# Performance work log

Measured on AMD Instinct MI355X. Metric: run time of the kernel, lower is better.

## Reference

```python
import jax, jax.numpy as jnp
import numpy as np


def setup_inputs() -> dict:
    key = jax.random.key(0)
    k1, k2, k3, k4 = jax.random.split(key, 4)
    B, C, H, W = 8, 3, 1024, 2048
    M, h, w = 32, H // 8, W // 8
    img = jax.random.uniform(k1, (B, C, H, W), dtype=jnp.float32)
    planar_masks = jax.random.normal(k2, (B, M, h, w), dtype=jnp.float32)
    disp = jax.random.uniform(k3, (B, h, w), dtype=jnp.float32) * 0.9 + 0.1
    K = jnp.array([[721.5, 0.0, w / 2.0], [0.0, 721.5, h / 2.0], [0.0, 0.0, 1.0]], dtype=jnp.float32)
    intrs = jnp.tile(K[None], (B, 1, 1))
    baseline = jax.random.uniform(k4, (B,), dtype=jnp.float32) * 0.4 + 0.3
    return {"img": img, "planar_masks": planar_masks, "disp": disp, "intrs": intrs, "baseline": baseline}


def reference(img, planar_masks, disp, intrs, baseline):
    B, C, H, W = img.shape
    _, M, h, w = planar_masks.shape
    dt = img.dtype

    # disp -> depth (b,h,w)
    focal = (intrs[:, 0, 0] + intrs[:, 1, 1]) * 0.5
    depth = baseline[:, None, None] * focal[:, None, None] / (disp * 2048.0)

    # depth -> normals via 3x3 Sobel-style central differences, zero padding
    dp = jnp.pad(depth, ((0, 0), (1, 1), (1, 1)))
    gx = 0.5 * (dp[:, 1:-1, 2:] - dp[:, 1:-1, :-2])
    gy = 0.5 * (dp[:, 2:, 1:-1] - dp[:, :-2, 1:-1])
    dir_map = jnp.stack([-gx, -gy, jnp.ones_like(gx)], axis=1)  # (B,3,h,w)
    normal = dir_map / jnp.sqrt(jnp.sum(dir_map ** 2, axis=1, keepdims=True))

    # softmax-weighted per-plane depth/normal (faithful torch .view memory layout)
    wts = jax.nn.softmax(planar_masks.reshape(B, M, h * w), axis=-1)  # (B,M,hw)
    flat_depth = depth.reshape(B, h * w, 1)
    flat_normal = normal.reshape(B, h * w, 3)  # channel-major flatten, as in source
    planar_depth = wts @ flat_depth   # (B,M,1)
    planar_normal = wts @ flat_normal  # (B,M,3)

    # per-plane homographies H = K (R - t n^T / d) K^-1
    R = jnp.broadcast_to(jnp.eye(3, dtype=dt), (B, 3, 3))
    t = jnp.zeros((B, 3, 1), dt).at[:, 2, 0].set(-baseline)
    K_inv = jnp.linalg.inv(intrs)
    tn = t[:, None] @ planar_normal[:, :, None, :]            # (B,M,3,3)
    H_cal = R[:, None] - tn / planar_depth[..., None]
    Hm = intrs[:, None] @ H_cal @ K_inv[:, None]              # (B,M,3,3)

    img_p = img.reshape(B, C, h, 8, w, 8).mean(axis=(3, 5))  # (B,C,h,w)

    # affine_grid (align_corners=True) with the top 2 rows of H
    ys = jnp.linspace(-1.0, 1.0, h, dtype=dt)
    xs = jnp.linspace(-1.0, 1.0, w, dtype=dt)
    gyy, gxx = jnp.meshgrid(ys, xs, indexing="ij")
    base = jnp.stack([gxx, gyy, jnp.ones_like(gxx)], axis=-1)  # (h,w,3)
    grid = jnp.einsum("bmij,hwj->bmhwi", Hm[:, :, :2, :], base)  # (B,M,h,w,2)

    # bilinear grid_sample, zeros padding, align_corners=True
    ix = (grid[..., 0] + 1.0) * (w - 1) * 0.5
    iy = (grid[..., 1] + 1.0) * (h - 1) * 0.5
    x0 = jnp.floor(ix)
    y0 = jnp.floor(iy)
    wx1 = ix - x0
    wy1 = iy - y0
    imgT = img_p.transpose(0, 2, 3, 1)  # (B,h,w,C)
    bidx = jnp.arange(B)[:, None, None, None]

    def corner(xf, yf):
        valid = (xf >= 0) & (xf <= w - 1) & (yf >= 0) & (yf <= h - 1)
        xi = jnp.clip(xf, 0, w - 1).astype(jnp.int32)
        yi = jnp.clip(yf, 0, h - 1).astype(jnp.int32)
        return imgT[bidx, yi, xi] * valid[..., None].astype(dt)  # (B,M,h,w,C)

    warp = (corner(x0, y0) * ((1 - wx1) * (1 - wy1))[..., None]
            + corner(x0 + 1, y0) * (wx1 * (1 - wy1))[..., None]
            + corner(x0, y0 + 1) * ((1 - wx1) * wy1)[..., None]
            + corner(x0 + 1, y0 + 1) * (wx1 * wy1)[..., None])  # (B,M,h,w,C)

    blend = jax.nn.softmax(planar_masks, axis=1)  # (B,M,h,w)
    return jnp.einsum("bmhwc,bmhw->bchw", warp, blend)
```

## Files before the change

### kernel.cpp

```cpp
#include <hip/hip_runtime.h>
#include <math.h>

#define Bq   8
#define Cc   3
#define Hh   128
#define Ww   256
#define Mm   32
#define HW   (Hh*Ww)
#define HIMG 1024
#define WIMG 2048

__global__ void k_dn(const float* __restrict__ disp,
                     const float* __restrict__ intrs,
                     const float* __restrict__ baseline,
                     float* __restrict__ depth,
                     float* __restrict__ normal) {
    int idx = blockIdx.x * 256 + threadIdx.x;
    int b = idx >> 15;
    int p = idx & (HW - 1);
    int y = p >> 8;
    int x = p & (Ww - 1);
    float focal = 0.5f * (intrs[b * 9 + 0] + intrs[b * 9 + 4]);
    float k = baseline[b] * focal * (1.0f / 2048.0f);
    const float* db = disp + (size_t)b * HW;
    float Dc  = k / db[p];
    float Dxm = (x > 0)      ? k / db[p - 1]  : 0.0f;
    float Dxp = (x < Ww - 1) ? k / db[p + 1]  : 0.0f;
    float Dym = (y > 0)      ? k / db[p - Ww] : 0.0f;
    float Dyp = (y < Hh - 1) ? k / db[p + Ww] : 0.0f;
    float gx = 0.5f * (Dxp - Dxm);
    float gy = 0.5f * (Dyp - Dym);
    float invn = 1.0f / sqrtf(gx * gx + gy * gy + 1.0f);
    depth[idx] = Dc;
    float* nb = normal + (size_t)b * 3 * HW;
    nb[p]          = -gx * invn;
    nb[HW + p]     = -gy * invn;
    nb[2 * HW + p] =  invn;
}

__global__ __launch_bounds__(512) void k_pool_planes(
        const float* __restrict__ img, float4* __restrict__ img_p,
        const float* __restrict__ masks,
        const float* __restrict__ depth, const float* __restrict__ normal,
        const float* __restrict__ intrs, const float* __restrict__ baseline,
        float* __restrict__ hm) {
    int blk = blockIdx.x;
    int tid = threadIdx.x;
    __shared__ float lds[5][8];
    if (blk < Bq * Mm) {
        int bm = blk;
        int b = bm >> 5;
        const float4* mp = (const float4*)(masks + (size_t)bm * HW);
        const float4* dp = (const float4*)(depth + (size_t)b * HW);
        const float4* np = (const float4*)(normal + (size_t)b * 3 * HW);
        int lane = tid & 63, wid = tid >> 6;

        float se = 0.f, sd = 0.f, s0 = 0.f, s1 = 0.f, s2 = 0.f;
        #pragma unroll 4
        for (int kk = 0; kk < HW / 4 / 512; kk++) {
            int i = tid + kk * 512;
            float4 mk  = mp[i];
            float4 d4  = dp[i];
            float4 n0v = np[3 * i], n1v = np[3 * i + 1], n2v = np[3 * i + 2];
            float e0 = __expf(mk.x), e1 = __expf(mk.y);
            float e2 = __expf(mk.z), e3 = __expf(mk.w);
            se += (e0 + e1) + (e2 + e3);
            sd = fmaf(e0, d4.x, fmaf(e1, d4.y, fmaf(e2, d4.z, fmaf(e3, d4.w, sd))));
            s0 = fmaf(e0, n0v.x, fmaf(e1, n0v.w, fmaf(e2, n1v.z, fmaf(e3, n2v.y, s0))));
            s1 = fmaf(e0, n0v.y, fmaf(e1, n1v.x, fmaf(e2, n1v.w, fmaf(e3, n2v.z, s1))));
            s2 = fmaf(e0, n0v.z, fmaf(e1, n1v.y, fmaf(e2, n2v.x, fmaf(e3, n2v.w, s2))));
        }
        float vals[5] = {se, sd, s0, s1, s2};
        #pragma unroll
        for (int j = 0; j < 5; j++) {
            float v = vals[j];
            #pragma unroll
            for (int off = 32; off; off >>= 1) v += __shfl_down(v, off, 64);
            if (lane == 0) lds[j][wid] = v;
        }
        __syncthreads();

        if (tid == 0) {
            float t[5];
            #pragma unroll
            for (int j = 0; j < 5; j++) {
                float r = 0.f;
                #pragma unroll
                for (int i = 0; i < 8; i++) r += lds[j][i];
                t[j] = r;
            }
            float inv_se = 1.0f / t[0];
            float pd = t[1] * inv_se;
            float n0 = t[2] * inv_se, n1 = t[3] * inv_se, n2 = t[4] * inv_se;
            const float* Km = intrs + b * 9;
            float a = Km[0], bb = Km[1], c = Km[2];
            float d = Km[3], e  = Km[4], f = Km[5];
            float g = Km[6], h2 = Km[7], i = Km[8];
            float det = a * (e * i - f * h2) - bb * (d * i - f * g) + c * (d * h2 - e * g);
            float invd = 1.0f / det;
            float ki[9] = {(e * i - f * h2) * invd, (c * h2 - bb * i) * invd, (bb * f - c * e) * invd,
                           (f * g - d * i) * invd, (a * i - c * g) * invd,  (c * d - a * f) * invd,
                           (d * h2 - e * g) * invd, (bb * g - a * h2) * invd, (a * e - bb * d) * invd};
            float s = baseline[b] / pd;
            float A[9] = {1.f, 0.f, 0.f, 0.f, 1.f, 0.f, s * n0, s * n1, 1.0f + s * n2};
            float T[9];
            #pragma unroll
            for (int r = 0; r < 3; r++)
                #pragma unroll
                for (int cc = 0; cc < 3; cc++)
                    T[r * 3 + cc] = Km[r * 3 + 0] * A[cc] + Km[r * 3 + 1] * A[3 + cc] + Km[r * 3 + 2] * A[6 + cc];
            #pragma unroll
            for (int r = 0; r < 2; r++)
                #pragma unroll
                for (int cc = 0; cc < 3; cc++)
                    hm[bm * 6 + r * 3 + cc] = T[r * 3 + 0] * ki[cc] + T[r * 3 + 1] * ki[3 + cc] + T[r * 3 + 2] * ki[6 + cc];
        }
    } else {
        int pb = blk - Bq * Mm;
        int b = pb >> 6;
        int y = ((pb & 63) << 1) | (tid >> 8);
        int x = tid & 255;
        float s[3];
        #pragma unroll
        for (int c = 0; c < 3; c++) {
            const float* base = img + ((size_t)(b * 3 + c) * HIMG + (size_t)y * 8) * WIMG + x * 8;
            float acc = 0.f;
            #pragma unroll
            for (int r = 0; r < 8; r++) {
                float4 u = *(const float4*)(base + (size_t)r * WIMG);
                float4 v = *(const float4*)(base + (size_t)r * WIMG + 4);
                acc += u.x + u.y + u.z + u.w + v.x + v.y + v.z + v.w;
            }
            s[c] = acc * (1.0f / 64.0f);
        }
        img_p[((size_t)(b * Hh + y)) * Ww + x] = make_float4(s[0], s[1], s[2], 0.f);
    }
}

__global__ __launch_bounds__(512) void k_blend(const float* __restrict__ masks,
                        const float* __restrict__ hm,
                        const float4* __restrict__ img_p,
                        float* __restrict__ out) {
    int bi = blockIdx.x;
    int b = bi >> 7;
    int y = bi & (Hh - 1);
    int tid = threadIdx.x;
    int x = tid & (Ww - 1);
    int half = tid >> 8;
    __shared__ float hs[Mm * 6];
    __shared__ float part[4][Ww];
    if (tid < Mm * 6) hs[tid] = hm[b * Mm * 6 + tid];
    __syncthreads();

    const float* mp = masks + (size_t)b * Mm * HW + (size_t)(half * 16) * HW
                    + (size_t)y * Ww + x;
    float mv[16];
    #pragma unroll
    for (int m = 0; m < 16; m++) mv[m] = mp[(size_t)m * HW];

    float xn = (2.0f * x - (float)(Ww - 1)) * (1.0f / (float)(Ww - 1));
    float yn = (2.0f * y - (float)(Hh - 1)) * (1.0f / (float)(Hh - 1));
    const float4* ip = img_p + (size_t)b * HW;
    const float* hb = hs + half * 16 * 6;

    float se = 0.f, a0 = 0.f, a1 = 0.f, a2 = 0.f;
    #pragma unroll 4
    for (int m = 0; m < 16; m++) {
        float e = __expf(mv[m]);
        se += e;
        float gx = fmaf(hb[m * 6 + 0], xn, fmaf(hb[m * 6 + 1], yn, hb[m * 6 + 2]));
        float gy = fmaf(hb[m * 6 + 3], xn, fmaf(hb[m * 6 + 4], yn, hb[m * 6 + 5]));
        float ix = (gx + 1.0f) * ((float)(Ww - 1) * 0.5f);
        float iy = (gy + 1.0f) * ((float)(Hh - 1) * 0.5f);
        float x0f = floorf(ix), y0f = floorf(iy);
        float wx1 = ix - x0f, wy1 = iy - y0f;
        float wx0 = 1.0f - wx1, wy0 = 1.0f - wy1;
        int x0i = (int)x0f, y0i = (int)y0f;
        float vx0 = ((unsigned)x0i       < (unsigned)Ww) ? wx0 : 0.0f;
        float vx1 = ((unsigned)(x0i + 1) < (unsigned)Ww) ? wx1 : 0.0f;
        float vy0 = ((unsigned)y0i       < (unsigned)Hh) ? wy0 * e : 0.0f;
        float vy1 = ((unsigned)(y0i + 1) < (unsigned)Hh) ? wy1 * e : 0.0f;
        int xc0 = min(max(x0i, 0), Ww - 1);
        int xc1 = min(max(x0i + 1, 0), Ww - 1);
        int r0 = min(max(y0i, 0), Hh - 1) * Ww;
        int r1 = min(max(y0i + 1, 0), Hh - 1) * Ww;
        float4 t00 = ip[r0 + xc0];
        float4 t10 = ip[r0 + xc1];
        float4 t01 = ip[r1 + xc0];
        float4 t11 = ip[r1 + xc1];
        float w00 = vx0 * vy0, w10 = vx1 * vy0;
        float w01 = vx0 * vy1, w11 = vx1 * vy1;
        a0 = fmaf(w00, t00.x, fmaf(w10, t10.x, fmaf(w01, t01.x, fmaf(w11, t11.x, a0))));
        a1 = fmaf(w00, t00.y, fmaf(w10, t10.y, fmaf(w01, t01.y, fmaf(w11, t11.y, a1))));
        a2 = fmaf(w00, t00.z, fmaf(w10, t10.z, fmaf(w01, t01.z, fmaf(w11, t11.z, a2))));
    }
    if (half) {
        part[0][x] = se; part[1][x] = a0; part[2][x] = a1; part[3][x] = a2;
    }
    __syncthreads();
    if (!half) {
        se += part[0][x]; a0 += part[1][x]; a1 += part[2][x]; a2 += part[3][x];
        float inv = 1.0f / se;
        int o = y * Ww + x;
        float* ob = out + (size_t)b * 3 * HW;
        ob[o]          = a0 * inv;
        ob[HW + o]     = a1 * inv;
        ob[2 * HW + o] = a2 * inv;
    }
}

extern "C" void kernel_launch(void* const* d_in, const int* in_sizes, int n_in,
                              void* d_out, int out_size, void* d_ws, size_t ws_size,
                              hipStream_t stream) {
    const float* img      = (const float*)d_in[0];
    const float* masks    = (const float*)d_in[1];
    const float* disp     = (const float*)d_in[2];
    const float* intrs    = (const float*)d_in[3];
    const float* baseline = (const float*)d_in[4];
    float* out = (float*)d_out;

    float* depth  = (float*)d_ws;
    float* normal = depth + (size_t)Bq * HW;
    float* hm     = normal + (size_t)Bq * 3 * HW;
    float4* img_p = (float4*)(hm + (size_t)Bq * Mm * 6);

    hipLaunchKernelGGL(k_dn, dim3(Bq * Hh), dim3(256), 0, stream,
                       disp, intrs, baseline, depth, normal);
    hipLaunchKernelGGL(k_pool_planes, dim3(Bq * Mm + Bq * Hh / 2), dim3(512), 0, stream,
                       img, img_p, masks, depth, normal, intrs, baseline, hm);
    hipLaunchKernelGGL(k_blend, dim3(Bq * Hh), dim3(512), 0, stream,
                       masks, hm, img_p, out);
}
```

Baseline: 335.1 us.

## Give each blend thread two rows over all planes; nontemporal loads in pooling

The blend kernel stops splitting the 32 planes across two half-blocks with a shared-memory reduction. Each thread now walks all planes for two adjacent output rows, with half as many blocks of 256 threads. This drops the __syncthreads partial-sum exchange and reuses the homography coefficients from shared memory for both rows. In exchange each thread does twice the serial work, so there are fewer waves to hide gather latency. The image pooling loads are also switched to nontemporal loads so the large streamed image does not pollute cache.

New measurement: 330.8 us. No clear change (-1.3%).

```diff
diff --git a/kernel.cpp b/kernel.cpp
--- a/kernel.cpp
+++ b/kernel.cpp
@@ -9,6 +9,8 @@
 #define HW   (Hh*Ww)
 #define HIMG 1024
 #define WIMG 2048
+
+typedef float f32x4 __attribute__((ext_vector_type(4)));
 
 __global__ void k_dn(const float* __restrict__ disp,
                      const float* __restrict__ intrs,
@@ -127,8 +129,8 @@
             float acc = 0.f;
             #pragma unroll
             for (int r = 0; r < 8; r++) {
-                float4 u = *(const float4*)(base + (size_t)r * WIMG);
-                float4 v = *(const float4*)(base + (size_t)r * WIMG + 4);
+                f32x4 u = __builtin_nontemporal_load((const f32x4*)(base + (size_t)r * WIMG));
+                f32x4 v = __builtin_nontemporal_load((const f32x4*)(base + (size_t)r * WIMG + 4));
                 acc += u.x + u.y + u.z + u.w + v.x + v.y + v.z + v.w;
             }
             s[c] = acc * (1.0f / 64.0f);
@@ -137,76 +139,77 @@
     }
 }
 
-__global__ __launch_bounds__(512) void k_blend(const float* __restrict__ masks,
+__global__ __launch_bounds__(256) void k_blend(const float* __restrict__ masks,
                         const float* __restrict__ hm,
                         const float4* __restrict__ img_p,
                         float* __restrict__ out) {
-    int bi = blockIdx.x;
-    int b = bi >> 7;
-    int y = bi & (Hh - 1);
-    int tid = threadIdx.x;
-    int x = tid & (Ww - 1);
-    int half = tid >> 8;
+    int blk = blockIdx.x;
+    int b = blk >> 6;
+    int y0 = (blk & 63) << 1;
+    int x = threadIdx.x;
     __shared__ float hs[Mm * 6];
-    __shared__ float part[4][Ww];
-    if (tid < Mm * 6) hs[tid] = hm[b * Mm * 6 + tid];
+    if (x < Mm * 6) hs[x] = hm[b * Mm * 6 + x];
     __syncthreads();
 
-    const float* mp = masks + (size_t)b * Mm * HW + (size_t)(half * 16) * HW
-                    + (size_t)y * Ww + x;
-    float mv[16];
-    #pragma unroll
-    for (int m = 0; m < 16; m++) mv[m] = mp[(size_t)m * HW];
-
-    float xn = (2.0f * x - (float)(Ww - 1)) * (1.0f / (float)(Ww - 1));
-    float yn = (2.0f * y - (float)(Hh - 1)) * (1.0f / (float)(Hh - 1));
+    const float* mp = masks + (size_t)b * Mm * HW + (size_t)y0 * Ww + x;
+    float xn  = (2.0f * x - (float)(Ww - 1)) * (1.0f / (float)(Ww - 1));
+    float yn0 = (2.0f * y0 - (float)(Hh - 1)) * (1.0f / (float)(Hh - 1));
+    float yn1 = (2.0f * (y0 + 1) - (float)(Hh - 1)) * (1.0f / (float)(Hh - 1));
     const float4* ip = img_p + (size_t)b * HW;
-    const float* hb = hs + half * 16 * 6;
-
-    float se = 0.f, a0 = 0.f, a1 = 0.f, a2 = 0.f;
+
+    float se0 = 0.f, a00 = 0.f, a01 = 0.f, a02 = 0.f;
+    float se1 = 0.f, a10 = 0.f, a11 = 0.f, a12 = 0.f;
     #pragma unroll 4
-    for (int m = 0; m < 16; m++) {
-        float e = __expf(mv[m]);
-        se += e;
-        float gx = fmaf(hb[m * 6 + 0], xn, fmaf(hb[m * 6 + 1], yn, hb[m * 6 + 2]));
-        float gy = fmaf(hb[m * 6 + 3], xn, fmaf(hb[m * 6 + 4], yn, hb[m * 6 + 5]));
-        float ix = (gx + 1.0f) * ((float)(Ww - 1) * 0.5f);
-        float iy = (gy + 1.0f) * ((float)(Hh - 1) * 0.5f);
-        float x0f = floorf(ix), y0f = floorf(iy);
-        float wx1 = ix - x0f, wy1 = iy - y0f;
-        float wx0 = 1.0f - wx1, wy0 = 1.0f - wy1;
-        int x0i = (int)x0f, y0i = (int)y0f;
-        float vx0 = ((unsigned)x0i       < (unsigned)Ww) ? wx0 : 0.0f;
-        float vx1 = ((unsigned)(x0i + 1) < (unsigned)Ww) ? wx1 : 0.0f;
-        float vy0 = ((unsigned)y0i       < (unsigned)Hh) ? wy0 * e : 0.0f;
-        float vy1 = ((unsigned)(y0i + 1) < (unsigned)Hh) ? wy1 * e : 0.0f;
-        int xc0 = min(max(x0i, 0), Ww - 1);
-        int xc1 = min(max(x0i + 1, 0), Ww - 1);
-        int r0 = min(max(y0i, 0), Hh - 1) * Ww;
-        int r1 = min(max(y0i + 1, 0), Hh - 1) * Ww;
-        float4 t00 = ip[r0 + xc0];
-        float4 t10 = ip[r0 + xc1];
-        float4 t01 = ip[r1 + xc0];
-        float4 t11 = ip[r1 + xc1];
-        float w00 = vx0 * vy0, w10 = vx1 * vy0;
-        float w01 = vx0 * vy1, w11 = vx1 * vy1;
-        a0 = fmaf(w00, t00.x, fmaf(w10, t10.x, fmaf(w01, t01.x, fmaf(w11, t11.x, a0))));
-        a1 = fmaf(w00, t00.y, fmaf(w10, t10.y, fmaf(w01, t01.y, fmaf(w11, t11.y, a1))));
-        a2 = fmaf(w00, t00.z, fmaf(w10, t10.z, fmaf(w01, t01.z, fmaf(w11, t11.z, a2))));
+    for (int m = 0; m < Mm; m++) {
+        float mv0 = mp[(size_t)m * HW];
+        float mv1 = mp[(size_t)m * HW + Ww];
+        float e0 = __expf(mv0);
+        float e1 = __expf(mv1);
+        se0 += e0;
+        se1 += e1;
+        float h0 = hs[m * 6 + 0], h1 = hs[m * 6 + 1], h2 = hs[m * 6 + 2];
+        float h3 = hs[m * 6 + 3], h4 = hs[m * 6 + 4], h5 = hs[m * 6 + 5];
+        #define ROWSAMPLE(YN, E, SA0, SA1, SA2) do {                                \
+            float gx = fmaf(h0, xn, fmaf(h1, (YN), h2));                            \
+            float gy = fmaf(h3, xn, fmaf(h4, (YN), h5));                            \
+            float ix = (gx + 1.0f) * ((float)(Ww - 1) * 0.5f);                      \
+            float iy = (gy + 1.0f) * ((float)(Hh - 1) * 0.5f);                      \
+            float x0f = floorf(ix), y0f = floorf(iy);                               \
+            float wx1 = ix - x0f, wy1 = iy - y0f;                                   \
+            float wx0 = 1.0f - wx1, wy0 = 1.0f - wy1;                               \
+            int x0i = (int)x0f, y0i = (int)y0f;                                     \
+            float vx0 = ((unsigned)x0i       < (unsigned)Ww) ? wx0 : 0.0f;          \
+            float vx1 = ((unsigned)(x0i + 1) < (unsigned)Ww) ? wx1 : 0.0f;          \
+            float vy0 = ((unsigned)y0i       < (unsigned)Hh) ? wy0 * (E) : 0.0f;    \
+            float vy1 = ((unsigned)(y0i + 1) < (unsigned)Hh) ? wy1 * (E) : 0.0f;    \
+            int xc0 = min(max(x0i, 0), Ww - 1);                                     \
+            int xc1 = min(max(x0i + 1, 0), Ww - 1);                                 \
+            int r0 = min(max(y0i, 0), Hh - 1) * Ww;                                 \
+            int r1 = min(max(y0i + 1, 0), Hh - 1) * Ww;                             \
+            float4 t00 = ip[r0 + xc0];                                              \
+            float4 t10 = ip[r0 + xc1];                                              \
+            float4 t01 = ip[r1 + xc0];                                              \
+            float4 t11 = ip[r1 + xc1];                                              \
+            float w00 = vx0 * vy0, w10 = vx1 * vy0;                                 \
+            float w01 = vx0 * vy1, w11 = vx1 * vy1;                                 \
+            SA0 = fmaf(w00, t00.x, fmaf(w10, t10.x, fmaf(w01, t01.x, fmaf(w11, t11.x, SA0)))); \
+            SA1 = fmaf(w00, t00.y, fmaf(w10, t10.y, fmaf(w01, t01.y, fmaf(w11, t11.y, SA1)))); \
+            SA2 = fmaf(w00, t00.z, fmaf(w10, t10.z, fmaf(w01, t01.z, fmaf(w11, t11.z, SA2)))); \
+        } while (0)
+        ROWSAMPLE(yn0, e0, a00, a01, a02);
+        ROWSAMPLE(yn1, e1, a10, a11, a12);
+        #undef ROWSAMPLE
     }
-    if (half) {
-        part[0][x] = se; part[1][x] = a0; part[2][x] = a1; part[3][x] = a2;
-    }
-    __syncthreads();
-    if (!half) {
-        se += part[0][x]; a0 += part[1][x]; a1 += part[2][x]; a2 += part[3][x];
-        float inv = 1.0f / se;
-        int o = y * Ww + x;
-        float* ob = out + (size_t)b * 3 * HW;
-        ob[o]          = a0 * inv;
-        ob[HW + o]     = a1 * inv;
-        ob[2 * HW + o] = a2 * inv;
-    }
+    int o = y0 * Ww + x;
+    float* ob = out + (size_t)b * 3 * HW;
+    float inv0 = 1.0f / se0;
+    ob[o]          = a00 * inv0;
+    ob[HW + o]     = a01 * inv0;
+    ob[2 * HW + o] = a02 * inv0;
+    float inv1 = 1.0f / se1;
+    ob[o + Ww]          = a10 * inv1;
+    ob[HW + o + Ww]     = a11 * inv1;
+    ob[2 * HW + o + Ww] = a12 * inv1;
 }
 
 extern "C" void kernel_launch(void* const* d_in, const int* in_sizes, int n_in,
@@ -228,6 +231,6 @@
                        disp, intrs, baseline, depth, normal);
     hipLaunchKernelGGL(k_pool_planes, dim3(Bq * Mm + Bq * Hh / 2), dim3(512), 0, stream,
                        img, img_p, masks, depth, normal, intrs, baseline, hm);
-    hipLaunchKernelGGL(k_blend, dim3(Bq * Hh), dim3(512), 0, stream,
+    hipLaunchKernelGGL(k_blend, dim3(Bq * Hh / 2), dim3(256), 0, stream,
                        masks, hm, img_p, out);
 }
```
